# Optimization experiments

Hardware: AMD Instinct MI355X
Metric: run time of the kernel (lower is better)

The kernel has to match this reference:

```python
import jax, jax.numpy as jnp
import numpy as np

L = 6                      # lmax = mmax (single resolution)
C = 128                    # sphere_channels
H = 256                    # hidden_channels
EC = 128                   # edge_channels
NG = 512                   # gaussian distance basis size
NC = (L + 1) ** 2          # 49 spherical coefficients
GP = 2 * (L + 1) ** 2      # 98 grid points
N_ATOMS = 800
N_EDGES = 8000
MAX_ELEM = 90
CUTOFF = 8.0
M_SIZES = [L - m + 1 for m in range(L + 1)]
MAXIN = L * C              # widest per-m SO2 input (m=1)


def _perm_np():
    # l-primary index of coefficient (l, m) is l*l + l + m
    idx = lambda l, m: l * l + l + m
    p = [idx(l, 0) for l in range(L + 1)]
    for m in range(1, L + 1):
        p += [idx(l, -m) for l in range(m, L + 1)]
        p += [idx(l, m) for l in range(m, L + 1)]
    return np.array(p)

_P = _perm_np()
PERM = jnp.array(_P)          # l-primary -> m-primary (x._m_primary)
INV_PERM = jnp.array(np.argsort(_P))  # m-primary -> l-primary (x._l_primary)


def silu(x):
    return x * jax.nn.sigmoid(x)


def setup_inputs() -> dict:
    key = jax.random.key(0)
    ks = iter(jax.random.split(key, 64))
    def nrm(shape, scale):
        return jax.random.normal(next(ks), shape, dtype=jnp.float32) * np.float32(scale)
    def lin(out_d, in_d):
        return nrm((out_d, in_d), 1.0 / np.sqrt(in_d))
    def so2_params(prefix):
        return {
            prefix + 'w_dist0': lin(H, EC), prefix + 'b_dist0': jnp.zeros((H,), jnp.float32),
            prefix + 'w1_m0': lin(H, M_SIZES[0] * C), prefix + 'w2_m0': lin(M_SIZES[0] * C, H),
            prefix + 'wdist_m': nrm((L, 2 * H, EC), 1.0 / np.sqrt(EC)),
            prefix + 'bdist_m': jnp.zeros((L, 2 * H), jnp.float32),
            prefix + 'w1r': nrm((L, H, MAXIN), 1.0 / np.sqrt(MAXIN)),
            prefix + 'w2r': nrm((L, MAXIN, H), 1.0 / np.sqrt(H)),
            prefix + 'w1i': nrm((L, H, MAXIN), 1.0 / np.sqrt(MAXIN)),
            prefix + 'w2i': nrm((L, MAXIN, H), 1.0 / np.sqrt(H)),
        }
    inp = dict(
        x=nrm((N_ATOMS, NC, C), 1.0),
        edge_distance=jax.random.uniform(next(ks), (N_EDGES,), jnp.float32, 0.5, CUTOFF),
        wigner=nrm((N_EDGES, NC, NC), 1.0 / np.sqrt(NC)),
        wigner_inv=nrm((N_EDGES, NC, NC), 1.0 / np.sqrt(NC)),
        to_grid_mat=nrm((GP, NC), 1.0 / np.sqrt(NC)),
        from_grid_mat=nrm((NC, GP), 1.0 / np.sqrt(GP)),
        w_dist1=lin(EC, NG), b_dist1=jnp.zeros((EC,), jnp.float32),
        src_emb=jax.random.uniform(next(ks), (MAX_ELEM, EC), jnp.float32, -0.001, 0.001),
        tgt_emb=jax.random.uniform(next(ks), (MAX_ELEM, EC), jnp.float32, -0.001, 0.001),
        w_edge1=lin(EC, EC), b_edge1=jnp.zeros((EC,), jnp.float32),
        ws1=lin(C, 2 * C), bs1=jnp.zeros((C,), jnp.float32),
        ws2=lin(C, C), bs2=jnp.zeros((C,), jnp.float32),
        ws3=lin(C, C), bs3=jnp.zeros((C,), jnp.float32),
        atomic_numbers=jax.random.randint(next(ks), (N_ATOMS,), 0, MAX_ELEM),
        edge_index=jax.random.randint(next(ks), (2, N_EDGES), 0, N_ATOMS),
    )
    inp.update(so2_params('s_'))
    inp.update(so2_params('t_'))
    return inp


def _so2_block(xr, x_edge, p):
    # SO2Block: m-primary reorder, m=0 gated MLP, per-m complex gated GEMMs, back to l-primary
    (w_dist0, b_dist0, w1_m0, w2_m0, wdist_m, bdist_m, w1r, w2r, w1i, w2i) = p
    E = xr.shape[0]
    xm = xr[:, PERM]                                   # [E, NC, C] m-primary
    n0 = M_SIZES[0]
    g0 = silu(x_edge @ w_dist0.T + b_dist0)            # [E, H]
    x0 = xm[:, :n0].reshape(E, n0 * C)
    x0 = ((x0 @ w1_m0.T) * g0) @ w2_m0.T
    outs = [x0.reshape(E, n0, C)]
    off = n0
    for m in range(1, L + 1):
        n = M_SIZES[m]; k = n * C
        blk = xm[:, off:off + 2 * n].reshape(E, 2, k)  # [E, 2(real/imag), n*C]
        ge = silu(x_edge @ wdist_m[m - 1].T + bdist_m[m - 1]).reshape(E, 2, H)
        xr_ = jnp.einsum('eik,hk->eih', blk, w1r[m - 1, :, :k]) * ge[:, 0:1]
        xr_ = jnp.einsum('eih,kh->eik', xr_, w2r[m - 1, :k])
        xi_ = jnp.einsum('eik,hk->eih', blk, w1i[m - 1, :, :k]) * ge[:, 1:2]
        xi_ = jnp.einsum('eih,kh->eik', xi_, w2i[m - 1, :k])
        out = jnp.stack([xr_[:, 0] - xi_[:, 1], xr_[:, 1] + xi_[:, 0]], axis=1)
        outs.append(out.reshape(E, 2 * n, C))
        off += 2 * n
    return jnp.concatenate(outs, axis=1)[:, INV_PERM]


def reference(x, edge_distance, wigner, wigner_inv, to_grid_mat, from_grid_mat,
              w_dist1, b_dist1, src_emb, tgt_emb, w_edge1, b_edge1,
              s_w_dist0, s_b_dist0, s_w1_m0, s_w2_m0, s_wdist_m, s_bdist_m,
              s_w1r, s_w2r, s_w1i, s_w2i,
              t_w_dist0, t_b_dist0, t_w1_m0, t_w2_m0, t_wdist_m, t_bdist_m,
              t_w1r, t_w2r, t_w1i, t_w2i,
              ws1, bs1, ws2, bs2, ws3, bs3,
              atomic_numbers, edge_index):
    # --- EdgeBlock ---
    offsets = jnp.linspace(0.0, CUTOFF, NG)
    coeff = np.float32(-0.5 / (CUTOFF / (NG - 1)) ** 2)
    basis = jnp.exp(coeff * (edge_distance[:, None] - offsets) ** 2)   # GaussianSmearing
    x_dist = basis @ w_dist1.T + b_dist1
    x_edge = silu(src_emb[atomic_numbers[edge_index[0]]]
                  + tgt_emb[atomic_numbers[edge_index[1]]] + x_dist)
    x_edge = silu(x_edge @ w_edge1.T + b_edge1)                        # [E, EC]
    # --- gather per-edge embeddings and rotate into edge frame ---
    x_src = jnp.einsum('eij,ejc->eic', wigner, x[edge_index[0]])
    x_tgt = jnp.einsum('eij,ejc->eic', wigner, x[edge_index[1]])
    # --- SO2 blocks ---
    x_src = _so2_block(x_src, x_edge, (s_w_dist0, s_b_dist0, s_w1_m0, s_w2_m0,
                                       s_wdist_m, s_bdist_m, s_w1r, s_w2r, s_w1i, s_w2i))
    x_tgt = _so2_block(x_tgt, x_edge, (t_w_dist0, t_b_dist0, t_w1_m0, t_w2_m0,
                                       t_wdist_m, t_bdist_m, t_w1r, t_w2r, t_w1i, t_w2i))
    msg = x_src + x_tgt
    # --- grid activation (x._grid_act) ---
    g = silu(jnp.einsum('gi,eic->egc', to_grid_mat, msg))
    msg = jnp.einsum('ig,egc->eic', from_grid_mat, g)
    # --- rotate back and aggregate (x._rotate_inv, x._reduce_edge) ---
    msg = jnp.einsum('eij,ejc->eic', wigner_inv, msg)
    x_msg = jax.ops.segment_sum(msg, edge_index[1], num_segments=x.shape[0])
    # --- LayerBlock point-wise spherical nonlinearity on the grid ---
    gx = jnp.einsum('gi,nic->ngc', to_grid_mat, x)
    gm = jnp.einsum('gi,nic->ngc', to_grid_mat, x_msg)
    g = jnp.concatenate([gx, gm], axis=-1)            # [N, GP, 2C]
    g = silu(g @ ws1.T + bs1)
    g = silu(g @ ws2.T + bs2)
    g = g @ ws3.T + bs3
    return jnp.einsum('ig,ngc->nic', from_grid_mat, g)
```

## Files before the change

kernel.cpp:

```cpp
#include <hip/hip_runtime.h>
#include <string.h>

#define EN 8000
#define AN 800

typedef __attribute__((ext_vector_type(8))) short bf16x8;
typedef __attribute__((ext_vector_type(4))) float f32x4;
typedef unsigned short ushort_t;
typedef unsigned int uint32;

__constant__ int c_perm[49] = {
  0,2,6,12,20,30,42,
  1,5,11,19,29,41,
  3,7,13,21,31,43,
  4,10,18,28,40,
  8,14,22,32,44,
  9,17,27,39,
  15,23,33,45,
  16,26,38,
  24,34,46,
  25,37,
  35,47,
  36,
  48
};

__device__ __forceinline__ float siluf(float x) { return x / (1.0f + __expf(-x)); }
__device__ __forceinline__ ushort_t f2bf(float f) {
  uint32 u = __float_as_uint(f);
  u += 0x7fff + ((u >> 16) & 1);
  return (ushort_t)(u >> 16);
}
__device__ __forceinline__ float bf2f(ushort_t h) {
  return __uint_as_float(((uint32)h) << 16);
}
__device__ __forceinline__ void gld16(const void* g, void* l) {
  __builtin_amdgcn_global_load_lds(
      (const __attribute__((address_space(1))) void*)g,
      (__attribute__((address_space(3))) void*)l, 16, 0, 0);
}

__global__ __launch_bounds__(256) void k_build_b2b(
    const float* __restrict__ sw2r, const float* __restrict__ sw2i,
    const float* __restrict__ tw2r, const float* __restrict__ tw2i,
    ushort_t* __restrict__ dst)
{
  long long id = (long long)blockIdx.x * 256 + threadIdx.x;
  if (id >= 5505024LL) return;
  long long base = 0; int m = 1, k = 768;
  for (; m <= 6; ++m) {
    k = (7 - m) * 128;
    long long sz = 2LL * k * 1024;
    if (id < base + sz) break;
    base += sz;
  }
  long long rem = id - base;
  int p = (int)(rem / ((long long)k * 1024));
  int cj = (int)(rem - (long long)p * k * 1024);
  int c = cj >> 10, j = cj & 1023;
  int q = j >> 8, jj = j & 255;
  const float sgn = (q & 1) ? (p ? 1.f : -1.f) : 1.f;
  const float* src = (q < 2) ? (q == 0 ? sw2r : sw2i) : (q == 2 ? tw2r : tw2i);
  dst[id] = f2bf(sgn * src[(long long)(m - 1) * 196608 + c * 256 + jj]);
}

__global__ __launch_bounds__(256) void k_build_bgcat(
    const float* __restrict__ sw0, const float* __restrict__ tw0,
    const float* __restrict__ sw4, const float* __restrict__ tw4,
    const float* __restrict__ sb0, const float* __restrict__ tb0b,
    const float* __restrict__ sbd, const float* __restrict__ tbd,
    ushort_t* __restrict__ w, float* __restrict__ b)
{
  int id = blockIdx.x * 256 + threadIdx.x;
  if (id < 851968) {
    int r = id >> 7, c = id & 127;
    float v;
    if (r < 256) v = sw0[r * 128 + c];
    else if (r < 512) v = tw0[(r - 256) * 128 + c];
    else {
      int rr = r - 512, m = rr >> 10, q = rr & 1023;
      v = (q < 512) ? sw4[m * 65536 + q * 128 + c] : tw4[m * 65536 + (q - 512) * 128 + c];
    }
    w[id] = f2bf(v);
    return;
  }
  id -= 851968;
  if (id < 6656) {
    float v;
    if (id < 256) v = sb0[id];
    else if (id < 512) v = tb0b[id - 256];
    else {
      int rr = id - 512, m = rr >> 10, q = rr & 1023;
      v = (q < 512) ? sbd[m * 512 + q] : tbd[m * 512 + (q - 512)];
    }
    b[id] = v;
  }
}

__global__ __launch_bounds__(256) void k_build_b20b(
    const float* __restrict__ sw3, const float* __restrict__ tw3,
    ushort_t* __restrict__ b20)
{
  int id = blockIdx.x * 256 + threadIdx.x;
  if (id >= 458752) return;
  int cc = id >> 9, j = id & 511;
  b20[id] = f2bf((j < 256) ? sw3[cc * 256 + j] : tw3[cc * 256 + (j - 256)]);
}

__global__ __launch_bounds__(256) void k_build_s1m(
    const float* __restrict__ sw6, const float* __restrict__ sw8,
    const float* __restrict__ tw6, const float* __restrict__ tw8,
    ushort_t* __restrict__ dst)
{
  long long id = (long long)blockIdx.x * 256 + threadIdx.x;
  if (id >= 2752512LL) return;
  long long base = 0; int m = 1, k = 768;
  for (; m <= 6; ++m) {
    k = (7 - m) * 128;
    long long sz = 1024LL * k;
    if (id < base + sz) break;
    base += sz;
  }
  long long rem = id - base;
  int s = (int)(rem / (512LL * k));
  int rr = (int)(rem - (long long)s * 512 * k);
  int r = rr / k, c = rr - r * k;
  const float* src = (r < 256) ? (s ? tw6 : sw6) : (s ? tw8 : sw8);
  int r0 = (r < 256) ? r : r - 256;
  dst[id] = f2bf(src[(long long)(m - 1) * 196608 + r0 * 768 + c]);
}

__global__ __launch_bounds__(256) void k_cvt(
    const float* __restrict__ src, ushort_t* __restrict__ dst, int n)
{
  int id = blockIdx.x * 256 + threadIdx.x;
  if (id < n) dst[id] = f2bf(src[id]);
}

__global__ __launch_bounds__(256) void k_build_tg(
    const float* __restrict__ tg, ushort_t* __restrict__ dst)
{
  int id = blockIdx.x * 256 + threadIdx.x;
  if (id >= 98 * 49) return;
  int r = id / 49, s = id - r * 49;
  dst[id] = f2bf(tg[r * 49 + c_perm[s]]);
}

__global__ __launch_bounds__(256) void k_xT(
    const float* __restrict__ x, ushort_t* __restrict__ xbT)
{
  __shared__ __align__(16) float xs[49 * 128];
  const int a = blockIdx.x, t = threadIdx.x;
  const float4* src = (const float4*)(x + (long long)a * 6272);
  float4* d = (float4*)xs;
  for (int i = t; i < 1568; i += 256) d[i] = src[i];
  __syncthreads();
  ushort_t* o = xbT + (long long)a * 8192;
  int c = t >> 1;
  int jg = (t & 1) << 2;
  #pragma unroll
  for (int u = 0; u < 4; ++u) {
    int g = jg + u;
    bf16x8 v = (bf16x8)0;
    #pragma unroll
    for (int j = 0; j < 8; ++j) {
      int jj = (g << 3) + j;
      if (jj < 49) v[j] = (short)f2bf(xs[jj * 128 + c]);
    }
    *(bf16x8*)&o[(c << 6) + (g << 3)] = v;
  }
}

__global__ __launch_bounds__(256) void k_basis(
    const float* __restrict__ dist, ushort_t* __restrict__ basis)
{
  int id = blockIdx.x * 256 + threadIdx.x;
  if (id >= EN * 512) return;
  int e = id >> 9, g = id & 511;
  const float step = 8.0f / 511.0f;
  const float coeff = -2040.0078125f;
  float df = dist[e] - (float)g * step;
  basis[id] = f2bf(expf(coeff * df * df));
}

__global__ __launch_bounds__(256) void k_emb(
    const float* __restrict__ src_emb, const float* __restrict__ tgt_emb,
    const int* __restrict__ anum, const int* __restrict__ eidx,
    const float* __restrict__ xd, ushort_t* __restrict__ out)
{
  int id = blockIdx.x * 256 + threadIdx.x;
  if (id >= EN * 128) return;
  int e = id >> 7, c = id & 127;
  int a0 = anum[eidx[e]], a1 = anum[eidx[EN + e]];
  out[id] = f2bf(siluf(src_emb[a0 * 128 + c] + tgt_emb[a1 * 128 + c] + xd[id]));
}

__global__ __launch_bounds__(256) void k_rot2(
    const float* __restrict__ wig, const ushort_t* __restrict__ xbT,
    const int* __restrict__ srcl, const int* __restrict__ tgtl,
    ushort_t* __restrict__ osrc, ushort_t* __restrict__ otgt)
{
  __shared__ short Ws[4096];
  __shared__ short Xs[8192];
  __shared__ short Xt[8192];
  const int e = blockIdx.x, tid = threadIdx.x;
  const int lane = tid & 63, wave = tid >> 6;
  const float* wge = wig + (long long)e * 2401;
  #pragma unroll
  for (int t = 0; t < 2; ++t) {
    int ci = (t << 8) + tid;
    int row = ci >> 3, g = ci & 7;
    bf16x8 v = (bf16x8)0;
    if (row < 49) {
      const float* wr = wge + c_perm[row] * 49;
      #pragma unroll
      for (int j = 0; j < 8; ++j) {
        int col = (g << 3) + j;
        if (col < 49) v[j] = (short)f2bf(wr[col]);
      }
    }
    *(bf16x8*)&Ws[(row << 6) + ((g ^ (row & 7)) << 3)] = v;
  }
  const int as = srcl[e], at = tgtl[e];
  const ushort_t* xsg = xbT + (long long)as * 8192;
  const ushort_t* xtg = xbT + (long long)at * 8192;
  #pragma unroll
  for (int t = 0; t < 4; ++t) {
    int ci = (t << 8) + tid;
    int row = ci >> 3, g = ci & 7;
    int ofs = (row << 6) + ((g ^ (row & 7)) << 3);
    *(bf16x8*)&Xs[ofs] = *(const bf16x8*)&xsg[ci << 3];
    *(bf16x8*)&Xt[ofs] = *(const bf16x8*)&xtg[ci << 3];
  }
  __syncthreads();
  const short* Xb = (wave >> 1) ? Xt : Xs;
  ushort_t* ob = ((wave >> 1) ? otgt : osrc) + (long long)e * 6272;
  const int ch = (wave & 1) << 6;
  const int fr = lane & 15, g = lane >> 4;
  f32x4 acc[4][4];
  #pragma unroll
  for (int i = 0; i < 4; ++i)
    #pragma unroll
    for (int j = 0; j < 4; ++j) acc[i][j] = (f32x4){0.f, 0.f, 0.f, 0.f};
  #pragma unroll
  for (int ks = 0; ks < 2; ++ks) {
    bf16x8 af[4], bfv[4];
    int lc = (ks << 2) + g;
    #pragma unroll
    for (int i = 0; i < 4; ++i) {
      int ra = (i << 4) + fr;
      af[i] = *(const bf16x8*)&Ws[(ra << 6) + ((lc ^ (ra & 7)) << 3)];
      int rb = ch + (i << 4) + fr;
      bfv[i] = *(const bf16x8*)&Xb[(rb << 6) + ((lc ^ (rb & 7)) << 3)];
    }
    #pragma unroll
    for (int i = 0; i < 4; ++i)
      #pragma unroll
      for (int j = 0; j < 4; ++j)
        acc[i][j] = __builtin_amdgcn_mfma_f32_16x16x32_bf16(af[i], bfv[j], acc[i][j], 0, 0, 0);
  }
  const int crl = (lane >> 4) << 2, ccl = lane & 15;
  #pragma unroll
  for (int i = 0; i < 4; ++i)
    #pragma unroll
    for (int r = 0; r < 4; ++r) {
      int q = (i << 4) + crl + r;
      if (q < 49) {
        #pragma unroll
        for (int j = 0; j < 4; ++j) {
          int col = ch + (j << 4) + ccl;
          ob[q * 128 + col] = f2bf(acc[i][j][r]);
        }
      }
    }
}

struct GemmP {
  const ushort_t* A; const ushort_t* A2; const ushort_t* B;
  const float* bias; const ushort_t* gate; void* C;
  int a_se, a_si, pair, asplit;
  int ldb;
  int gate_ofs;
  int c_se, c_si, c_ofs;
  int ihalf, act, c_bf16;
  int M, N, K;
  int ngx, wg_base;
};
struct Grouped { GemmP d[14]; int nd; };

__global__ __launch_bounds__(256) void gemm_g(Grouped G) {
  __shared__ short As[4096];
  __shared__ short Bs[4096];
  const int bid = blockIdx.x;
  int di = G.nd - 1;
  for (int i = 1; i < G.nd; ++i) if (bid < G.d[i].wg_base) { di = i - 1; break; }
  const GemmP p = G.d[di];
  const int local = bid - p.wg_base;
  const int bx = local % p.ngx, by = local / p.ngx;
  const int m0 = bx << 7, n0 = by << 7;

  const int tid = threadIdx.x;
  const int lane = tid & 63, wave = tid >> 6;
  const int gl = ((lane & 3) ^ ((lane >> 3) & 3)) << 3;
  const int grow = (wave << 4) + (lane >> 2);
  const int fr = lane & 15, fkg = lane >> 4;
  const int sxor = (fr >> 1) & 3;
  const int wm = (wave >> 1) << 6, wn = (wave & 1) << 6;

  f32x4 acc[4][4];
  #pragma unroll
  for (int i = 0; i < 4; ++i)
    #pragma unroll
    for (int j = 0; j < 4; ++j) acc[i][j] = (f32x4){0.f, 0.f, 0.f, 0.f};

  for (int k0 = 0; k0 < p.K; k0 += 32) {
    const ushort_t* Ap = p.A;
    int kk = k0;
    if (p.A2 && k0 >= p.asplit) { Ap = p.A2; kk = k0 - p.asplit; }
    #pragma unroll
    for (int t = 0; t < 2; ++t) {
      int r = m0 + (t << 6) + grow;
      long long base = p.pair
          ? (long long)(r >> 1) * p.a_se + (long long)(r & 1) * p.a_si
          : (long long)r * p.a_se;
      gld16(Ap + base + kk + gl, &As[(t << 11) + (wave << 9)]);
      int rn = n0 + (t << 6) + grow;
      gld16(p.B + (long long)rn * p.ldb + k0 + gl, &Bs[(t << 11) + (wave << 9)]);
    }
    __syncthreads();
    bf16x8 af[4], bfv[4];
    #pragma unroll
    for (int i = 0; i < 4; ++i) {
      int ra = wm + (i << 4) + fr;
      int rb = wn + (i << 4) + fr;
      af[i]  = *(const bf16x8*)&As[(ra << 5) + ((fkg ^ sxor) << 3)];
      bfv[i] = *(const bf16x8*)&Bs[(rb << 5) + ((fkg ^ sxor) << 3)];
    }
    #pragma unroll
    for (int i = 0; i < 4; ++i)
      #pragma unroll
      for (int j = 0; j < 4; ++j)
        acc[i][j] = __builtin_amdgcn_mfma_f32_16x16x32_bf16(af[i], bfv[j], acc[i][j], 0, 0, 0);
    __syncthreads();
  }

  const int crl = (lane >> 4) << 2, ccl = lane & 15;
  #pragma unroll
  for (int mi = 0; mi < 4; ++mi) {
    #pragma unroll
    for (int r = 0; r < 4; ++r) {
      int gr = m0 + wm + mi * 16 + crl + r;
      if (gr >= p.M) continue;
      long long e; int ii;
      if (p.pair) { e = gr >> 1; ii = gr & 1; } else { e = gr; ii = 0; }
      const ushort_t* grw = p.gate ? p.gate + e * 6656 + p.gate_ofs : nullptr;
      #pragma unroll
      for (int ni = 0; ni < 4; ++ni) {
        int gc = n0 + wn + ni * 16 + ccl;
        if (gc >= p.N) continue;
        float v = acc[mi][ni][r];
        if (p.bias) v += p.bias[gc];
        if (p.act)  v = siluf(v);
        if (grw)    v *= bf2f(grw[gc]);
        int par = (p.ihalf && gc >= 256) ? (1 - ii) : ii;
        long long co = e * (long long)p.c_se + (long long)par * p.c_si + p.c_ofs + gc;
        if (p.c_bf16) ((ushort_t*)p.C)[co] = f2bf(v);
        else          ((float*)p.C)[co] = v;
      }
    }
  }
}

struct GridP {
  const float* A; const ushort_t* B; void* C; const float* bias;
  int b_ib, c_ib;
  int M, K, permA, act, c_bf16;
};

#define LDW 40

__global__ __launch_bounds__(256) void gridmm(GridP p) {
  __shared__ short As[128 * LDW];
  __shared__ short Bs[128 * LDW];
  const int e = blockIdx.x;
  const int tid = threadIdx.x;
  const int srow = tid >> 1, sk = (tid & 1) << 4;
  const int lane = tid & 63, wave = tid >> 6;
  const int wm = (wave >> 1) << 6, wn = (wave & 1) << 6;
  const int fr = lane & 15, fk = (lane >> 4) << 3;

  f32x4 acc[4][4];
  #pragma unroll
  for (int i = 0; i < 4; ++i)
    #pragma unroll
    for (int j = 0; j < 4; ++j) acc[i][j] = (f32x4){0.f, 0.f, 0.f, 0.f};

  const ushort_t* bp0 = p.B + (long long)e * p.b_ib;

  for (int k0 = 0; k0 < p.K; k0 += 32) {
    {
      bf16x8 lo = (bf16x8)0, hi = (bf16x8)0;
      if (srow < p.M) {
        const float* ar = p.A + srow * p.K;
        #pragma unroll
        for (int j = 0; j < 8; ++j) {
          int col = k0 + sk + j;
          float v = 0.f;
          if (col < p.K) v = ar[p.permA ? c_perm[col] : col];
          lo[j] = (short)f2bf(v);
        }
        #pragma unroll
        for (int j = 0; j < 8; ++j) {
          int col = k0 + sk + 8 + j;
          float v = 0.f;
          if (col < p.K) v = ar[p.permA ? c_perm[col] : col];
          hi[j] = (short)f2bf(v);
        }
      }
      *(bf16x8*)&As[srow * LDW + sk] = lo;
      *(bf16x8*)&As[srow * LDW + sk + 8] = hi;
    }
    {
      const int c = tid & 127, kq = tid >> 7;
      #pragma unroll
      for (int i = 0; i < 8; ++i) {
        int kk = kq * 16 + i * 2;
        int k1 = k0 + kk, k2 = k1 + 1;
        uint32 v0 = (k1 < p.K) ? (uint32)bp0[(long long)k1 * 128 + c] : 0u;
        uint32 v1 = (k2 < p.K) ? (uint32)bp0[(long long)k2 * 128 + c] : 0u;
        *(uint32*)&Bs[c * LDW + kk] = v0 | (v1 << 16);
      }
    }
    __syncthreads();
    bf16x8 af[4], bfv[4];
    #pragma unroll
    for (int i = 0; i < 4; ++i) {
      af[i]  = *(const bf16x8*)(&As[(wm + i * 16 + fr) * LDW + fk]);
      bfv[i] = *(const bf16x8*)(&Bs[(wn + i * 16 + fr) * LDW + fk]);
    }
    #pragma unroll
    for (int i = 0; i < 4; ++i)
      #pragma unroll
      for (int j = 0; j < 4; ++j)
        acc[i][j] = __builtin_amdgcn_mfma_f32_16x16x32_bf16(af[i], bfv[j], acc[i][j], 0, 0, 0);
    __syncthreads();
  }

  const int crl = (lane >> 4) << 2, ccl = lane & 15;
  #pragma unroll
  for (int mi = 0; mi < 4; ++mi) {
    #pragma unroll
    for (int r = 0; r < 4; ++r) {
      int gr = wm + mi * 16 + crl + r;
      if (gr >= p.M) continue;
      #pragma unroll
      for (int ni = 0; ni < 4; ++ni) {
        int c = wn + ni * 16 + ccl;
        float v = acc[mi][ni][r];
        if (p.bias) v += p.bias[c];
        if (p.act)  v = siluf(v);
        long long co = (long long)e * p.c_ib + gr * 128 + c;
        if (p.c_bf16) ((ushort_t*)p.C)[co] = f2bf(v);
        else          ((float*)p.C)[co] = v;
      }
    }
  }
}

#define SWZ8(cg, r) (((cg) ^ ((r) & 7)) & 7)
#define SWZ16(cg, r) (((cg) & 8) | (((cg) ^ (r)) & 7))

__global__ __launch_bounds__(256, 2) void k_grid(
    const ushort_t* __restrict__ tgb, const ushort_t* __restrict__ fgb,
    const float* __restrict__ wigv, const ushort_t* __restrict__ msgp,
    ushort_t* __restrict__ msg3)
{
  __shared__ short Abuf[8192];
  __shared__ short Bsh[8192];
  __shared__ short Ps[16384];
  const int e = blockIdx.x, tid = threadIdx.x;
  const int lane = tid & 63, wv = tid >> 6;
  const int fr = lane & 15, fk = (lane >> 4) << 3;
  const int crl = (lane >> 4) << 2, ccl = lane & 15;
  const ushort_t* me = msgp + (long long)e * 6272;

  for (int gid = tid; gid < 896; gid += 256) {
    int r = gid >> 3, cg = gid & 7;
    bf16x8 v = (bf16x8)0;
    if (r < 98) {
      #pragma unroll
      for (int j = 0; j < 8; ++j) {
        int col = (cg << 3) + j;
        if (col < 49) v[j] = (short)tgb[r * 49 + col];
      }
    }
    *(bf16x8*)&Abuf[(r << 6) + (SWZ8(cg, r) << 3)] = v;
  }
  for (int gid = tid; gid < 1024; gid += 256) {
    int kg = gid >> 7, c = gid & 127;
    bf16x8 v = (bf16x8)0;
    #pragma unroll
    for (int j = 0; j < 8; ++j) {
      int k = (kg << 3) + j;
      if (k < 49) v[j] = (short)me[k * 128 + c];
    }
    *(bf16x8*)&Bsh[(c << 6) + (SWZ8(kg, c) << 3)] = v;
  }
  {
    int c = tid >> 1, gg = 14 + (tid & 1);
    *(bf16x8*)&Ps[(c << 7) + (SWZ16(gg, c) << 3)] = (bf16x8)0;
  }
  __syncthreads();

  {
    f32x4 acc[7][2];
    #pragma unroll
    for (int i = 0; i < 7; ++i) { acc[i][0] = (f32x4){0,0,0,0}; acc[i][1] = (f32x4){0,0,0,0}; }
    #pragma unroll
    for (int k0 = 0; k0 < 64; k0 += 32) {
      int cg = (k0 + fk) >> 3;
      int br0 = ((2 * wv) << 4) + fr, br1 = ((2 * wv + 1) << 4) + fr;
      bf16x8 bf0 = *(const bf16x8*)&Bsh[(br0 << 6) + (SWZ8(cg, br0) << 3)];
      bf16x8 bf1 = *(const bf16x8*)&Bsh[(br1 << 6) + (SWZ8(cg, br1) << 3)];
      #pragma unroll
      for (int rt = 0; rt < 7; ++rt) {
        int ar = (rt << 4) + fr;
        bf16x8 af = *(const bf16x8*)&Abuf[(ar << 6) + (SWZ8(cg, ar) << 3)];
        acc[rt][0] = __builtin_amdgcn_mfma_f32_16x16x32_bf16(af, bf0, acc[rt][0], 0, 0, 0);
        acc[rt][1] = __builtin_amdgcn_mfma_f32_16x16x32_bf16(af, bf1, acc[rt][1], 0, 0, 0);
      }
    }
    #pragma unroll
    for (int rt = 0; rt < 7; ++rt)
      #pragma unroll
      for (int cj = 0; cj < 2; ++cj) {
        int c = ((2 * wv + cj) << 4) + ccl;
        #pragma unroll
        for (int r = 0; r < 4; ++r) {
          int g = (rt << 4) + crl + r;
          Ps[(c << 7) + (SWZ16(g >> 3, c) << 3) + (g & 7)] =
              (short)f2bf(siluf(acc[rt][cj][r]));
        }
      }
  }
  __syncthreads();
  for (int gid = tid; gid < 1024; gid += 256) {
    int r = gid >> 4, cg = gid & 15;
    bf16x8 v = (bf16x8)0;
    if (r < 49) {
      #pragma unroll
      for (int j = 0; j < 8; ++j) {
        int col = (cg << 3) + j;
        if (col < 98) v[j] = (short)fgb[r * 98 + col];
      }
    }
    *(bf16x8*)&Abuf[(r << 7) + (SWZ16(cg, r) << 3)] = v;
  }
  __syncthreads();

  {
    f32x4 acc[4][2];
    #pragma unroll
    for (int i = 0; i < 4; ++i) { acc[i][0] = (f32x4){0,0,0,0}; acc[i][1] = (f32x4){0,0,0,0}; }
    #pragma unroll
    for (int k0 = 0; k0 < 128; k0 += 32) {
      int cg = (k0 + fk) >> 3;
      int br0 = ((2 * wv) << 4) + fr, br1 = ((2 * wv + 1) << 4) + fr;
      bf16x8 bf0 = *(const bf16x8*)&Ps[(br0 << 7) + (SWZ16(cg, br0) << 3)];
      bf16x8 bf1 = *(const bf16x8*)&Ps[(br1 << 7) + (SWZ16(cg, br1) << 3)];
      #pragma unroll
      for (int rt = 0; rt < 4; ++rt) {
        int ar = (rt << 4) + fr;
        bf16x8 af = *(const bf16x8*)&Abuf[(ar << 7) + (SWZ16(cg, ar) << 3)];
        acc[rt][0] = __builtin_amdgcn_mfma_f32_16x16x32_bf16(af, bf0, acc[rt][0], 0, 0, 0);
        acc[rt][1] = __builtin_amdgcn_mfma_f32_16x16x32_bf16(af, bf1, acc[rt][1], 0, 0, 0);
      }
    }
    #pragma unroll
    for (int rt = 0; rt < 4; ++rt)
      #pragma unroll
      for (int cj = 0; cj < 2; ++cj) {
        int c = ((2 * wv + cj) << 4) + ccl;
        #pragma unroll
        for (int r = 0; r < 4; ++r) {
          int q = (rt << 4) + crl + r;
          Bsh[(c << 6) + (SWZ8(q >> 3, c) << 3) + (q & 7)] = (short)f2bf(acc[rt][cj][r]);
        }
      }
  }
  __syncthreads();
  {
    const float* we = wigv + (long long)e * 2401;
    for (int gid = tid; gid < 512; gid += 256) {
      int r = gid >> 3, cg = gid & 7;
      bf16x8 v = (bf16x8)0;
      if (r < 49) {
        #pragma unroll
        for (int j = 0; j < 8; ++j) {
          int col = (cg << 3) + j;
          if (col < 49) v[j] = (short)f2bf(we[r * 49 + col]);
        }
      }
      *(bf16x8*)&Abuf[(r << 6) + (SWZ8(cg, r) << 3)] = v;
    }
  }
  __syncthreads();

  {
    f32x4 acc[4][2];
    #pragma unroll
    for (int i = 0; i < 4; ++i) { acc[i][0] = (f32x4){0,0,0,0}; acc[i][1] = (f32x4){0,0,0,0}; }
    #pragma unroll
    for (int k0 = 0; k0 < 64; k0 += 32) {
      int cg = (k0 + fk) >> 3;
      int br0 = ((2 * wv) << 4) + fr, br1 = ((2 * wv + 1) << 4) + fr;
      bf16x8 bf0 = *(const bf16x8*)&Bsh[(br0 << 6) + (SWZ8(cg, br0) << 3)];
      bf16x8 bf1 = *(const bf16x8*)&Bsh[(br1 << 6) + (SWZ8(cg, br1) << 3)];
      #pragma unroll
      for (int rt = 0; rt < 4; ++rt) {
        int ar = (rt << 4) + fr;
        bf16x8 af = *(const bf16x8*)&Abuf[(ar << 6) + (SWZ8(cg, ar) << 3)];
        acc[rt][0] = __builtin_amdgcn_mfma_f32_16x16x32_bf16(af, bf0, acc[rt][0], 0, 0, 0);
        acc[rt][1] = __builtin_amdgcn_mfma_f32_16x16x32_bf16(af, bf1, acc[rt][1], 0, 0, 0);
      }
    }
    ushort_t* oe = msg3 + (long long)e * 6272;
    #pragma unroll
    for (int rt = 0; rt < 4; ++rt)
      #pragma unroll
      for (int r = 0; r < 4; ++r) {
        int gi = (rt << 4) + crl + r;
        if (gi < 49) {
          #pragma unroll
          for (int cj = 0; cj < 2; ++cj) {
            int c = ((2 * wv + cj) << 4) + ccl;
            oe[gi * 128 + c] = f2bf(acc[rt][cj][r]);
          }
        }
      }
  }
}

__global__ __launch_bounds__(256) void k_zeroi(int* __restrict__ p, int n) {
  int id = blockIdx.x * 256 + threadIdx.x;
  if (id < n) p[id] = 0;
}

__global__ __launch_bounds__(256) void k_deg(
    const int* __restrict__ tgt, int* __restrict__ deg) {
  int e = blockIdx.x * 256 + threadIdx.x;
  if (e < EN) atomicAdd(&deg[tgt[e]], 1);
}

__global__ __launch_bounds__(1024) void k_prefix(
    const int* __restrict__ deg, int* __restrict__ base) {
  __shared__ int s[1024];
  int t = threadIdx.x;
  s[t] = (t < AN) ? deg[t] : 0;
  __syncthreads();
  for (int ofs = 1; ofs < 1024; ofs <<= 1) {
    int u = (t >= ofs) ? s[t - ofs] : 0;
    __syncthreads();
    s[t] += u;
    __syncthreads();
  }
  if (t < AN) base[t + 1] = s[t];
  if (t == 0) base[0] = 0;
}

__global__ __launch_bounds__(256) void k_fill(
    const int* __restrict__ tgt, const int* __restrict__ base,
    int* __restrict__ list) {
  const int a = blockIdx.x, t = threadIdx.x;
  const int lane = t & 63, w = t >> 6;
  __shared__ int wtot[4];
  __shared__ int runbase;
  if (t == 0) runbase = base[a];
  __syncthreads();
  for (int i0 = 0; i0 < EN; i0 += 256) {
    int e = i0 + t;
    bool m = (e < EN) && (tgt[e] == a);
    unsigned long long bal = __ballot(m);
    if (lane == 0) wtot[w] = __popcll(bal);
    __syncthreads();
    int wbase = 0;
    for (int j = 0; j < w; ++j) wbase += wtot[j];
    int tot = wtot[0] + wtot[1] + wtot[2] + wtot[3];
    if (m) {
      int off = __popcll(bal & ((1ull << lane) - 1ull));
      list[runbase + wbase + off] = e;
    }
    __syncthreads();
    if (t == 0) runbase += tot;
    __syncthreads();
  }
}

__global__ __launch_bounds__(256) void k_gather(
    const ushort_t* __restrict__ msg3, const int* __restrict__ base,
    const int* __restrict__ list, float* __restrict__ xmsg,
    int e0, int ce, int accum)
{
  const int a = blockIdx.x, part = blockIdx.y, t = threadIdx.x;
  const int b0 = base[a], b1 = base[a + 1];
  const int ofs = part * 784;
  float acc[4] = {0.f, 0.f, 0.f, 0.f};
  for (int i = b0; i < b1; ++i) {
    int e = list[i];
    if (e < e0 || e >= e0 + ce) continue;
    const ushort_t* m = msg3 + (long long)(e - e0) * 6272 + ofs;
    #pragma unroll
    for (int u = 0; u < 4; ++u) {
      int idx = t + (u << 8);
      if (idx < 784) acc[u] += bf2f(m[idx]);
    }
  }
  float* o = xmsg + (long long)a * 6272 + ofs;
  #pragma unroll
  for (int u = 0; u < 4; ++u) {
    int idx = t + (u << 8);
    if (idx < 784) {
      if (accum) o[idx] += acc[u]; else o[idx] = acc[u];
    }
  }
}

extern "C" void kernel_launch(void* const* d_in, const int* in_sizes, int n_in,
                              void* d_out, int out_size, void* d_ws, size_t ws_size,
                              hipStream_t stream) {
  const float* x         = (const float*)d_in[0];
  const float* edist     = (const float*)d_in[1];
  const float* wigner    = (const float*)d_in[2];
  const float* wiginv    = (const float*)d_in[3];
  const float* to_grid   = (const float*)d_in[4];
  const float* from_grid = (const float*)d_in[5];
  const float* w_dist1   = (const float*)d_in[6];
  const float* b_dist1   = (const float*)d_in[7];
  const float* src_emb   = (const float*)d_in[8];
  const float* tgt_emb   = (const float*)d_in[9];
  const float* w_edge1   = (const float*)d_in[10];
  const float* b_edge1   = (const float*)d_in[11];
  const float* ws1       = (const float*)d_in[12];
  const float* bs1       = (const float*)d_in[13];
  const float* ws2       = (const float*)d_in[14];
  const float* bs2       = (const float*)d_in[15];
  const float* ws3       = (const float*)d_in[16];
  const float* bs3       = (const float*)d_in[17];
  const int*   anum      = (const int*)d_in[18];
  const int*   eidx      = (const int*)d_in[19];
  const float* sw[10]; const float* tw[10];
  for (int i = 0; i < 10; ++i) {
    sw[i] = (const float*)d_in[20 + i];
    tw[i] = (const float*)d_in[30 + i];
  }
  float* outp = (float*)d_out;

  char* wsb = (char*)d_ws;
  size_t off = 0;
  auto alloc = [&](long long nbytes) {
    char* p = wsb + off; off += (size_t)((nbytes + 63) & ~63LL); return p;
  };
  ushort_t* x_edge  = (ushort_t*)alloc((8000LL + 128) * 128 * 2);
  ushort_t* b2ab    = (ushort_t*)alloc(5505024LL * 2);
  ushort_t* bgcw    = (ushort_t*)alloc(851968LL * 2);
  float*    bgcb    = (float*)alloc(6656 * 4);
  ushort_t* b20b    = (ushort_t*)alloc(458752LL * 2);
  ushort_t* s1m0b   = (ushort_t*)alloc(458752LL * 2);
  ushort_t* s1mb    = (ushort_t*)alloc(2752512LL * 2);
  ushort_t* wd1b    = (ushort_t*)alloc(65536 * 2);
  ushort_t* we1b    = (ushort_t*)alloc(16384 * 2);
  ushort_t* ws1b    = (ushort_t*)alloc(32768 * 2);
  ushort_t* ws2b    = (ushort_t*)alloc(16384 * 2);
  ushort_t* ws3b    = (ushort_t*)alloc(16384 * 2);
  ushort_t* tgb     = (ushort_t*)alloc(4802 * 2);
  ushort_t* fgb     = (ushort_t*)alloc(4802 * 2);
  float*    xmsg    = (float*)alloc(5017600LL * 4);
  ushort_t* xmsgb   = (ushort_t*)alloc((5017600LL + 16384) * 2);
  ushort_t* xb      = (ushort_t*)alloc((5017600LL + 16384) * 2);
  ushort_t* xbT     = (ushort_t*)alloc(6553600LL * 2);
  ushort_t* basis   = (ushort_t*)alloc((8000LL + 128) * 512 * 2);
  float*    x_dist  = (float*)alloc(1024000LL * 4);
  ushort_t* x_distb = (ushort_t*)alloc((8000LL + 128) * 128 * 2);
  int*      deg     = (int*)alloc(800 * 4);
  int*      sbase   = (int*)alloc(801 * 4);
  int*      elist   = (int*)alloc(8000 * 4);
  const size_t fixedB = off;
  char* arena = wsb + off;

  static const int ces[6] = {8000, 4000, 2000, 1000, 500, 250};
  static const int cas[6] = {800, 800, 800, 400, 200, 100};
  int ce = 250, ca = 100;
  for (int i = 0; i < 6; ++i) {
    long long ne = (long long)ces[i] * 76544 + 64LL * 50688;
    long long na = (long long)cas[i] * 87808 + 64LL * 512;
    long long need = (long long)fixedB + (ne > na ? ne : na);
    if (need <= (long long)ws_size) { ce = ces[i]; ca = cas[i]; break; }
  }

  char* ap = arena;
  ushort_t* xrot_s = (ushort_t*)ap;  ap += (long long)(ce + 64) * 12544;
  ushort_t* xrot_t = (ushort_t*)ap;  ap += (long long)(ce + 64) * 12544;
  ushort_t* tb0    = (ushort_t*)ap;  ap += (long long)(ce + 64) * 1024;
  ushort_t* tbm    = (ushort_t*)ap;  ap += (long long)(ce + 64) * 24576;
  ushort_t* msgp   = (ushort_t*)ap;  ap += (long long)ce * 12544;
  ushort_t* gate   = (ushort_t*)ap;
  ushort_t* msg3   = (ushort_t*)arena;
  char* bp = arena;
  ushort_t* hb = (ushort_t*)bp;  bp += (long long)ca * 49 * 256;
  ushort_t* g1 = (ushort_t*)bp;  bp += ((long long)ca * 98 + 64) * 256;
  ushort_t* g2 = (ushort_t*)bp;  bp += ((long long)ca * 98 + 64) * 256;
  ushort_t* g3 = (ushort_t*)bp;

  long long ofs2[7][2], s1ofs[7][2];
  { long long cur = 0, cur1 = 0;
    for (int m = 1; m <= 6; ++m) {
      int k = (7 - m) * 128;
      ofs2[m][0] = cur; cur += (long long)k * 1024;
      ofs2[m][1] = cur; cur += (long long)k * 1024;
      s1ofs[m][0] = cur1; cur1 += 512LL * k;
      s1ofs[m][1] = cur1; cur1 += 512LL * k;
    } }

  auto D0 = []() { GemmP p; memset(&p, 0, sizeof(p)); p.asplit = 1 << 30; return p; };
  auto finalize = [&](Grouped& G) {
    int base = 0;
    for (int i = 0; i < G.nd; ++i) {
      GemmP& p = G.d[i];
      p.ngx = (p.M + 127) >> 7;
      int ngy = (p.N + 127) >> 7;
      p.wg_base = base;
      base += p.ngx * ngy;
    }
    gemm_g<<<base, 256, 0, stream>>>(G);
  };
  auto run1 = [&](GemmP p) { Grouped G; G.d[0] = p; G.nd = 1; finalize(G); };
  auto rungrid = [&](const float* A, int M, int K, int permA,
                     const ushort_t* B, int b_ib, void* C, int c_ib,
                     const float* bias, int act, int c_bf16, int nb) {
    GridP p;
    p.A = A; p.B = B; p.C = C; p.bias = bias;
    p.b_ib = b_ib; p.c_ib = c_ib;
    p.M = M; p.K = K; p.permA = permA; p.act = act; p.c_bf16 = c_bf16;
    gridmm<<<nb, 256, 0, stream>>>(p);
  };
  auto cvt = [&](const float* s, ushort_t* d, int n) {
    k_cvt<<<(n + 255) / 256, 256, 0, stream>>>(s, d, n);
  };

  k_build_b2b<<<(5505024 + 255) / 256, 256, 0, stream>>>(sw[7], sw[9], tw[7], tw[9], b2ab);
  k_build_bgcat<<<(858624 + 255) / 256, 256, 0, stream>>>(
      sw[0], tw[0], sw[4], tw[4], sw[1], tw[1], sw[5], tw[5], bgcw, bgcb);
  k_build_b20b<<<(458752 + 255) / 256, 256, 0, stream>>>(sw[3], tw[3], b20b);
  k_build_s1m<<<(2752512 + 255) / 256, 256, 0, stream>>>(sw[6], sw[8], tw[6], tw[8], s1mb);
  cvt(sw[2], s1m0b, 229376);
  cvt(tw[2], s1m0b + 229376, 229376);
  cvt(w_dist1, wd1b, 65536);
  cvt(w_edge1, we1b, 16384);
  cvt(ws1, ws1b, 32768);
  cvt(ws2, ws2b, 16384);
  cvt(ws3, ws3b, 16384);
  cvt(from_grid, fgb, 4802);
  k_build_tg<<<(4802 + 255) / 256, 256, 0, stream>>>(to_grid, tgb);
  cvt(x, xb, 5017600);
  k_xT<<<AN, 256, 0, stream>>>(x, xbT);

  k_zeroi<<<4, 256, 0, stream>>>(deg, 800);
  k_deg<<<(EN + 255) / 256, 256, 0, stream>>>(eidx + EN, deg);
  k_prefix<<<1, 1024, 0, stream>>>(deg, sbase);
  k_fill<<<AN, 256, 0, stream>>>(eidx + EN, sbase, elist);

  k_basis<<<(EN * 512 + 255) / 256, 256, 0, stream>>>(edist, basis);
  { GemmP p = D0();
    p.A = basis; p.a_se = 512; p.B = wd1b; p.ldb = 512; p.bias = b_dist1;
    p.C = x_dist; p.c_se = 128; p.M = EN; p.N = 128; p.K = 512;
    run1(p); }
  k_emb<<<(EN * 128 + 255) / 256, 256, 0, stream>>>(src_emb, tgt_emb, anum, eidx,
                                                    x_dist, x_distb);
  { GemmP p = D0();
    p.A = x_distb; p.a_se = 128; p.B = we1b; p.ldb = 128; p.bias = b_edge1;
    p.act = 1; p.C = x_edge; p.c_se = 128; p.c_bf16 = 1;
    p.M = EN; p.N = 128; p.K = 128;
    run1(p); }

  static const int offq[7] = {0, 7, 19, 29, 37, 43, 47};

  for (int e0 = 0; e0 < EN; e0 += ce) {
    const int c = ce;
    k_rot2<<<c, 256, 0, stream>>>(wigner + (long long)e0 * 2401, xbT,
                                  eidx + e0, eidx + EN + e0, xrot_s, xrot_t);
    { GemmP p = D0();
      p.A = x_edge + (long long)e0 * 128; p.a_se = 128;
      p.B = bgcw; p.ldb = 128; p.bias = bgcb; p.act = 1;
      p.C = gate; p.c_se = 6656; p.c_bf16 = 1;
      p.M = c; p.N = 6656; p.K = 128;
      run1(p); }
    { Grouped G; G.nd = 14;
      for (int s = 0; s < 2; ++s) {
        GemmP p = D0();
        p.A = s ? xrot_t : xrot_s; p.a_se = 6272;
        p.B = s1m0b + (long long)s * 229376; p.ldb = 896;
        p.gate = gate; p.gate_ofs = s * 256;
        p.C = tb0; p.c_se = 512; p.c_ofs = s * 256; p.c_bf16 = 1;
        p.M = c; p.N = 256; p.K = 896;
        G.d[s] = p;
      }
      int di = 2;
      for (int m = 1; m <= 6; ++m) {
        const int k = (7 - m) * 128, off2 = offq[m];
        for (int s = 0; s < 2; ++s) {
          GemmP p = D0();
          p.A = (s ? xrot_t : xrot_s) + off2 * 128;
          p.a_se = 6272; p.a_si = k; p.pair = 1;
          p.B = s1mb + s1ofs[m][s]; p.ldb = k;
          p.gate = gate; p.gate_ofs = 512 + (m - 1) * 1024 + s * 512;
          p.C = tbm; p.c_se = 12288; p.c_si = 1024;
          p.c_ofs = (m - 1) * 2048 + s * 512;
          p.ihalf = 1; p.c_bf16 = 1;
          p.M = 2 * c; p.N = 512; p.K = k;
          G.d[di++] = p;
        }
      }
      finalize(G); }
    { Grouped G; G.nd = 13;
      { GemmP p = D0();
        p.A = tb0; p.a_se = 512;
        p.B = b20b; p.ldb = 512;
        p.C = msgp; p.c_se = 6272; p.c_bf16 = 1;
        p.M = c; p.N = 896; p.K = 512;
        G.d[0] = p; }
      int di = 1;
      for (int m = 1; m <= 6; ++m) {
        const int n = 7 - m, k = n * 128, off2 = offq[m];
        for (int pp = 0; pp < 2; ++pp) {
          GemmP p = D0();
          p.A = tbm + (m - 1) * 2048 + pp * 1024; p.a_se = 12288;
          p.B = b2ab + ofs2[m][pp]; p.ldb = 1024;
          p.C = msgp; p.c_se = 6272; p.c_ofs = (off2 + (pp ? n : 0)) * 128; p.c_bf16 = 1;
          p.M = c; p.N = k; p.K = 1024;
          G.d[di++] = p;
        }
      }
      finalize(G); }
    k_grid<<<c, 256, 0, stream>>>(tgb, fgb, wiginv + (long long)e0 * 2401, msgp, msg3);
    k_gather<<<dim3(AN, 8), 256, 0, stream>>>(msg3, sbase, elist, xmsg, e0, c, e0 > 0);
  }

  cvt(xmsg, xmsgb, 5017600);

  for (int a0 = 0; a0 < AN; a0 += ca) {
    { GemmP p = D0();
      p.A = xb + (long long)a0 * 6272; p.A2 = xmsgb + (long long)a0 * 6272;
      p.a_se = 128; p.asplit = 128;
      p.B = ws1b; p.ldb = 256;
      p.C = hb; p.c_se = 128; p.c_bf16 = 1;
      p.M = ca * 49; p.N = 128; p.K = 256;
      run1(p); }
    rungrid(to_grid, 98, 49, 0, hb, 6272, g1, 12544, bs1, 1, 1, ca);
    { GemmP p = D0();
      p.A = g1; p.a_se = 128;
      p.B = ws2b; p.ldb = 128; p.bias = bs2; p.act = 1;
      p.C = g2; p.c_se = 128; p.c_bf16 = 1;
      p.M = ca * 98; p.N = 128; p.K = 128;
      run1(p); }
    { GemmP p = D0();
      p.A = g2; p.a_se = 128;
      p.B = ws3b; p.ldb = 128; p.bias = bs3;
      p.C = g3; p.c_se = 128; p.c_bf16 = 1;
      p.M = ca * 98; p.N = 128; p.K = 128;
      run1(p); }
    rungrid(from_grid, 49, 98, 0, g3, 12544, outp + (long long)a0 * 6272, 6272,
            nullptr, 0, 0, ca);
  }
}
```

Before: 1.804 ms.

## Double-buffer LDS tiles in grouped GEMM to overlap global loads with MFMA

The grouped bf16 GEMM now uses two LDS buffers per operand. It prefetches the next K-tile's direct-to-LDS loads before computing on the current tile, and waits with a partial vmcnt instead of draining all loads each iteration. Per-row base addresses are also hoisted out of the K loop. This is meant to hide global load latency behind MFMA work, at the cost of doubling LDS per block, which may lower occupancy. The correctness of the vmcnt(4) count depends on gld16 issuing exactly one VMEM op per call.

```diff
diff --git a/kernel.cpp b/kernel.cpp
--- a/kernel.cpp
+++ b/kernel.cpp
@@ -289,8 +289,8 @@
 struct Grouped { GemmP d[14]; int nd; };
 
 __global__ __launch_bounds__(256) void gemm_g(Grouped G) {
-  __shared__ short As[4096];
-  __shared__ short Bs[4096];
+  __shared__ short As[8192];
+  __shared__ short Bs[8192];
   const int bid = blockIdx.x;
   int di = G.nd - 1;
   for (int i = 1; i < G.nd; ++i) if (bid < G.d[i].wg_base) { di = i - 1; break; }
@@ -313,35 +313,65 @@
     #pragma unroll
     for (int j = 0; j < 4; ++j) acc[i][j] = (f32x4){0.f, 0.f, 0.f, 0.f};
 
-  for (int k0 = 0; k0 < p.K; k0 += 32) {
+  long long abase;
+  {
+    int r0 = m0 + grow;
+    abase = p.pair
+        ? (long long)(r0 >> 1) * p.a_se + (long long)(r0 & 1) * p.a_si
+        : (long long)r0 * p.a_se;
+  }
+  long long abase2;
+  {
+    int r1 = m0 + 64 + grow;
+    abase2 = p.pair
+        ? (long long)(r1 >> 1) * p.a_se + (long long)(r1 & 1) * p.a_si
+        : (long long)r1 * p.a_se;
+  }
+  const long long bbase  = (long long)(n0 + grow) * p.ldb;
+  const long long bbase2 = (long long)(n0 + 64 + grow) * p.ldb;
+
+  const int nt = p.K >> 5;
+
+  auto STAGE = [&](int buf, int k0) {
     const ushort_t* Ap = p.A;
     int kk = k0;
     if (p.A2 && k0 >= p.asplit) { Ap = p.A2; kk = k0 - p.asplit; }
-    #pragma unroll
-    for (int t = 0; t < 2; ++t) {
-      int r = m0 + (t << 6) + grow;
-      long long base = p.pair
-          ? (long long)(r >> 1) * p.a_se + (long long)(r & 1) * p.a_si
-          : (long long)r * p.a_se;
-      gld16(Ap + base + kk + gl, &As[(t << 11) + (wave << 9)]);
-      int rn = n0 + (t << 6) + grow;
-      gld16(p.B + (long long)rn * p.ldb + k0 + gl, &Bs[(t << 11) + (wave << 9)]);
-    }
-    __syncthreads();
-    bf16x8 af[4], bfv[4];
-    #pragma unroll
-    for (int i = 0; i < 4; ++i) {
-      int ra = wm + (i << 4) + fr;
-      int rb = wn + (i << 4) + fr;
-      af[i]  = *(const bf16x8*)&As[(ra << 5) + ((fkg ^ sxor) << 3)];
-      bfv[i] = *(const bf16x8*)&Bs[(rb << 5) + ((fkg ^ sxor) << 3)];
-    }
-    #pragma unroll
-    for (int i = 0; i < 4; ++i)
-      #pragma unroll
-      for (int j = 0; j < 4; ++j)
-        acc[i][j] = __builtin_amdgcn_mfma_f32_16x16x32_bf16(af[i], bfv[j], acc[i][j], 0, 0, 0);
-    __syncthreads();
+    const int lofs = (buf << 12) + (wave << 9);
+    gld16(Ap + abase + kk + gl,        &As[lofs]);
+    gld16(p.B + bbase + k0 + gl,       &Bs[lofs]);
+    gld16(Ap + abase2 + kk + gl,       &As[lofs + 2048]);
+    gld16(p.B + bbase2 + k0 + gl,      &Bs[lofs + 2048]);
+  };
+
+  STAGE(0, 0);
+  int cur = 0;
+  for (int t = 0; t < nt; ++t) {
+    if (t + 1 < nt) {
+      STAGE(cur ^ 1, (t + 1) << 5);
+      asm volatile("s_waitcnt vmcnt(4)" ::: "memory");
+    } else {
+      asm volatile("s_waitcnt vmcnt(0)" ::: "memory");
+    }
+    __builtin_amdgcn_sched_barrier(0);
+    __builtin_amdgcn_s_barrier();
+    {
+      const int bofs = cur << 12;
+      bf16x8 af[4], bfv[4];
+      #pragma unroll
+      for (int i = 0; i < 4; ++i) {
+        int ra = wm + (i << 4) + fr;
+        int rb = wn + (i << 4) + fr;
+        af[i]  = *(const bf16x8*)&As[bofs + (ra << 5) + ((fkg ^ sxor) << 3)];
+        bfv[i] = *(const bf16x8*)&Bs[bofs + (rb << 5) + ((fkg ^ sxor) << 3)];
+      }
+      #pragma unroll
+      for (int i = 0; i < 4; ++i)
+        #pragma unroll
+        for (int j = 0; j < 4; ++j)
+          acc[i][j] = __builtin_amdgcn_mfma_f32_16x16x32_bf16(af[i], bfv[j], acc[i][j], 0, 0, 0);
+    }
+    __builtin_amdgcn_s_barrier();
+    cur ^= 1;
   }
 
   const int crl = (lane >> 4) << 2, ccl = lane & 15;
```

After: 1.760 ms. -2.5%, faster.
